# Optimization experiments

Measured on AMD Instinct MI355X. Metric: run time of the kernel, lower is better.

Reference implementation:

```python
import jax, jax.numpy as jnp
import numpy as np

BIG_NEG = -1000000000.0
B, N, X, D = 16, 32, 36, 2048
H = 512

def setup_inputs() -> dict:
    key = jax.random.key(0)
    ks = jax.random.split(key, 16)
    inp = {
        'fc_feats_target': jax.random.normal(ks[0], (B, 1, D), jnp.float32),
        'fc_feats_distr': jax.random.normal(ks[1], (B, N, D), jnp.float32),
        'att_feats_target': jax.random.normal(ks[2], (B, 1, X, D), jnp.float32),
        'att_feats_distr': jax.random.normal(ks[3], (B, N, X, D), jnp.float32),
        'att_masks_target': jax.random.randint(ks[4], (B, 1, X), 0, 2, jnp.int32),
        'att_masks_distr': jax.random.randint(ks[5], (B, N, X), 0, 2, jnp.int32),
        # scorer MLP params: Linear(2D->H), Linear(H->1)
        'W1': jax.random.normal(ks[6], (2 * D, H), jnp.float32) * 0.02,
        'b1': jnp.zeros((H,), jnp.float32),
        'W2': jax.random.normal(ks[7], (H, 1), jnp.float32) * 0.02,
        'b2': jnp.zeros((1,), jnp.float32),
        # bilinear weight, initialized to identity as in the module
        'Wbil': jnp.eye(D, dtype=jnp.float32),
        # object_scorer MLP params
        'oW1': jax.random.normal(ks[8], (2 * D, H), jnp.float32) * 0.02,
        'ob1': jnp.zeros((H,), jnp.float32),
        'oW2': jax.random.normal(ks[9], (H, 1), jnp.float32) * 0.02,
        'ob2': jnp.zeros((1,), jnp.float32),
    }
    return inp

def _mlp(x, W1, b1, W2, b2):
    h = jax.nn.relu(x @ W1 + b1)
    return (h @ W2 + b2)[..., 0]  # squeeze(-1)

def reference(fc_feats_target, fc_feats_distr, att_feats_target, att_feats_distr,
              att_masks_target, att_masks_distr,
              W1, b1, W2, b2, Wbil, oW1, ob1, oW2, ob2):
    # base scorer on global (fc) features
    ft = jnp.broadcast_to(fc_feats_target, fc_feats_distr.shape)  # [B,N,D]
    cat_feats = jnp.concatenate([ft, fc_feats_distr], axis=-1)    # [B,N,2D]
    scores = _mlp(cat_feats, W1, b1, W2, b2)                      # [B,N]

    # bilinear compatibility: einsum('bixd,biye,de->bixy') with target broadcast over i
    tproj = jnp.einsum('bxd,de->bxe', att_feats_target[:, 0], Wbil)        # [B,X,D]
    inners = jnp.einsum('bxd,biyd->bixy', tproj, att_feats_distr)          # [B,N,X,Y]

    mask_outer = (att_masks_target[:, 0][:, None, :, None]
                  * att_masks_distr[:, :, None, :])                        # [B,N,X,Y]
    inners = jnp.where(mask_outer > 0, inners, BIG_NEG)

    target_weights = jax.nn.softmax(jnp.max(inners, axis=3), axis=-1)      # [B,N,X]
    distr_weights = jax.nn.softmax(jnp.max(inners, axis=2), axis=-1)       # [B,N,Y]

    target_feats = jnp.einsum('bxd,bix->bid', att_feats_target[:, 0], target_weights)
    distr_feats = jnp.einsum('biyd,biy->bid', att_feats_distr, distr_weights)

    cat_att = jnp.concatenate([target_feats, distr_feats], axis=-1)        # [B,N,2D]
    scores = scores + _mlp(cat_att, oW1, ob1, oW2, ob2)

    return jax.nn.log_softmax(scores, axis=-1)  # [B,N]
```

## Files before the change

kernel.cpp:

```cpp
#include <hip/hip_runtime.h>
#include <math.h>

#define D_   2048
#define H_   512
#define K2D  4096
#define X_   36
#define NCOL 1152

#define Z_MLP 32
#define Z_TP  8

#define O_A   0u
#define O_B   9437184u
#define O_SB  11534336u
#define O_SO  11534848u
#define O_C   11536384u

typedef __attribute__((ext_vector_type(8))) short bf8_t;
typedef __attribute__((ext_vector_type(4))) float f4_t;

__device__ __forceinline__ unsigned short f2bf(float f) {
  unsigned u = __float_as_uint(f);
  unsigned r = u + 0x7FFFu + ((u >> 16) & 1u);
  return (unsigned short)(r >> 16);
}
__device__ __forceinline__ float bf2f(unsigned short h) {
  return __uint_as_float(((unsigned)h) << 16);
}

#define TSTR 40

__device__ __forceinline__ void cvt8(unsigned short* Hp, unsigned short* Lp,
                                     float4 a, float4 b) {
  __align__(16) unsigned short h[8], l[8];
  float x[8] = {a.x, a.y, a.z, a.w, b.x, b.y, b.z, b.w};
  #pragma unroll
  for (int j = 0; j < 8; j++) {
    h[j] = f2bf(x[j]);
    l[j] = f2bf(x[j] - bf2f(h[j]));
  }
  *(bf8_t*)Hp = *(bf8_t*)&h[0];
  *(bf8_t*)Lp = *(bf8_t*)&l[0];
}

__device__ __forceinline__ void cvt8v(bf8_t* H, bf8_t* L, float4 a, float4 b) {
  float x[8] = {a.x, a.y, a.z, a.w, b.x, b.y, b.z, b.w};
  bf8_t hh, ll;
  #pragma unroll
  for (int j = 0; j < 8; j++) {
    unsigned short h = f2bf(x[j]);
    hh[j] = (short)h;
    ll[j] = (short)f2bf(x[j] - bf2f(h));
  }
  *H = hh; *L = ll;
}

__global__ __launch_bounds__(256, 4) void gemm_mfma64(
    const float* __restrict__ A, const float* __restrict__ A2,
    const float* __restrict__ Bm, float* __restrict__ Cpart,
    int M, int N, int K, int kchunk, int amode)
{
  __shared__ __align__(16) unsigned short AsH[64 * TSTR], AsL[64 * TSTR];
  __shared__ __align__(16) unsigned short BsH[64 * TSTR], BsL[64 * TSTR];
  const int t  = threadIdx.x;
  const int m0 = blockIdx.y << 6;
  const int n0 = blockIdx.x << 6;
  const int k0 = blockIdx.z * kchunk;
  const int kend = k0 + kchunk;
  const int w  = t >> 6;
  const int ln = t & 15;
  const int qd = (t >> 4) & 3;
  const int wm = (w >> 1) << 5;
  const int wn = (w & 1) << 5;
  const int a_row = t >> 2;
  const int a_kq  = (t & 3) << 3;
  const int b_col = t & 63;
  const int b_kq  = (t >> 6) << 3;

  f4_t acc[2][2];
  #pragma unroll
  for (int i = 0; i < 2; i++)
    #pragma unroll
    for (int j = 0; j < 2; j++) acc[i][j] = (f4_t)0.f;

  float4 pa0, pa1;
  float  pb[8];

  auto loadA = [&](int kb) {
    int gr = m0 + a_row;
    int gk = kb + a_kq;
    pa0 = make_float4(0.f, 0.f, 0.f, 0.f);
    pa1 = pa0;
    if (gr < M) {
      const float* src;
      if (amode == 0) src = A + (size_t)gr * K + gk;
      else src = (gk < 2048) ? (A  + ((size_t)(gr >> 5) << 11) + gk)
                             : (A2 + ((size_t)gr << 11) + (gk - 2048));
      pa0 = *(const float4*)src;
      pa1 = *(const float4*)(src + 4);
    }
  };
  auto loadB = [&](int kb) {
    #pragma unroll
    for (int j = 0; j < 8; j++)
      pb[j] = Bm[(size_t)(kb + b_kq + j) * N + n0 + b_col];
  };

  loadA(k0); loadB(k0);

  for (int kb = k0; kb < kend; kb += 32) {
    __syncthreads();
    cvt8(&AsH[a_row * TSTR + a_kq], &AsL[a_row * TSTR + a_kq], pa0, pa1);
    cvt8(&BsH[b_col * TSTR + b_kq], &BsL[b_col * TSTR + b_kq],
         make_float4(pb[0], pb[1], pb[2], pb[3]),
         make_float4(pb[4], pb[5], pb[6], pb[7]));
    __syncthreads();
    if (kb + 32 < kend) { loadA(kb + 32); loadB(kb + 32); }
    bf8_t ah[2], al[2], bh[2], bl[2];
    #pragma unroll
    for (int fm = 0; fm < 2; fm++) {
      int r = (wm + (fm << 4) + ln) * TSTR + (qd << 3);
      ah[fm] = *(const bf8_t*)&AsH[r];
      al[fm] = *(const bf8_t*)&AsL[r];
    }
    #pragma unroll
    for (int fn = 0; fn < 2; fn++) {
      int r = (wn + (fn << 4) + ln) * TSTR + (qd << 3);
      bh[fn] = *(const bf8_t*)&BsH[r];
      bl[fn] = *(const bf8_t*)&BsL[r];
    }
    #pragma unroll
    for (int fm = 0; fm < 2; fm++)
      #pragma unroll
      for (int fn = 0; fn < 2; fn++) {
        acc[fm][fn] = __builtin_amdgcn_mfma_f32_16x16x32_bf16(ah[fm], bh[fn], acc[fm][fn], 0, 0, 0);
        acc[fm][fn] = __builtin_amdgcn_mfma_f32_16x16x32_bf16(ah[fm], bl[fn], acc[fm][fn], 0, 0, 0);
        acc[fm][fn] = __builtin_amdgcn_mfma_f32_16x16x32_bf16(al[fm], bh[fn], acc[fm][fn], 0, 0, 0);
      }
  }
  float* Cz = Cpart + (size_t)blockIdx.z * M * N;
  #pragma unroll
  for (int fm = 0; fm < 2; fm++) {
    #pragma unroll
    for (int reg = 0; reg < 4; reg++) {
      int gr = m0 + wm + (fm << 4) + (qd << 2) + reg;
      if (gr < M) {
        #pragma unroll
        for (int fn = 0; fn < 2; fn++)
          Cz[(size_t)gr * N + n0 + wn + (fn << 4) + ln] = acc[fm][fn][reg];
      }
    }
  }
}

__global__ __launch_bounds__(256) void reduce_tp(
    const float* __restrict__ tpp, unsigned short* __restrict__ tH,
    unsigned short* __restrict__ tL)
{
  int idx = blockIdx.x * 256 + threadIdx.x;
  const float4* p = (const float4*)tpp;
  float4 a = p[idx];
  #pragma unroll
  for (int z = 1; z < Z_TP; z++) {
    float4 b = p[idx + (size_t)z * 294912];
    a.x += b.x; a.y += b.y; a.z += b.z; a.w += b.w;
  }
  ushort4 h, l;
  h.x = f2bf(a.x); l.x = f2bf(a.x - bf2f(h.x));
  h.y = f2bf(a.y); l.y = f2bf(a.y - bf2f(h.y));
  h.z = f2bf(a.z); l.z = f2bf(a.z - bf2f(h.z));
  h.w = f2bf(a.w); l.w = f2bf(a.w - bf2f(h.w));
  ((ushort4*)tH)[idx] = h;
  ((ushort4*)tL)[idx] = l;
}

__global__ __launch_bounds__(256) void mlp_tail_z(
    const float* __restrict__ hp, const float* __restrict__ b1,
    const float* __restrict__ w2, const float* __restrict__ b2,
    float* __restrict__ out)
{
  int row = blockIdx.x;
  int t   = threadIdx.x;
  float v = 0.f;
  #pragma unroll
  for (int q = 0; q < 2; q++) {
    int h = t + (q << 8);
    float s = 0.f;
    #pragma unroll
    for (int z = 0; z < Z_MLP; z++)
      s += hp[(size_t)z * (H_ * 512) + (size_t)row * H_ + h];
    s += b1[h];
    v += fmaxf(s, 0.f) * w2[h];
  }
  #pragma unroll
  for (int off = 32; off > 0; off >>= 1) v += __shfl_down(v, off, 64);
  __shared__ float red[4];
  if ((t & 63) == 0) red[t >> 6] = v;
  __syncthreads();
  if (t == 0) out[row] = red[0] + red[1] + red[2] + red[3] + b2[0];
}

__global__ __launch_bounds__(256, 2) void attn_bi(
    const unsigned short* __restrict__ tH,
    const float* __restrict__ attd,
    const int* __restrict__ amt, const int* __restrict__ amd,
    const float* __restrict__ attt, float* __restrict__ cat)
{
  __shared__ float Sp[4][36][37];
  __shared__ int   mtv[36], mdv[36];
  __shared__ float mrow[36], mcol[36], twl[36], dwl[36];
  const int bi = blockIdx.x;
  const int b  = bi >> 5;
  const int t  = threadIdx.x;
  const int w  = t >> 6;
  const int ln = t & 15;
  const int qd = (t >> 4) & 3;
  if (t < 36) { mtv[t] = amt[b * 36 + t]; mdv[t] = amd[bi * 36 + t]; }

  const unsigned short* tLo = tH + 1179648;
  const int kw = (w << 9) + (qd << 3);
  const unsigned short* AH[3];
  const unsigned short* AL[3];
  const float* BP[3];
  #pragma unroll
  for (int f = 0; f < 3; f++) {
    int r = f * 16 + ln; if (r > 35) r = 35;
    size_t ao = ((size_t)b * X_ + r) * D_ + kw;
    AH[f] = tH  + ao;
    AL[f] = tLo + ao;
    BP[f] = attd + ((size_t)bi * X_ + r) * D_ + kw;
  }

  f4_t acc[3][3];
  #pragma unroll
  for (int i = 0; i < 3; i++)
    #pragma unroll
    for (int j = 0; j < 3; j++) acc[i][j] = (f4_t)0.f;

  bf8_t ah[3], al[3];
  float4 pb0[3], pb1[3];
  #pragma unroll
  for (int f = 0; f < 3; f++) {
    ah[f]  = *(const bf8_t*)AH[f];
    al[f]  = *(const bf8_t*)AL[f];
    pb0[f] = *(const float4*)BP[f];
    pb1[f] = *(const float4*)(BP[f] + 4);
  }

  for (int kk = 0; kk < 16; kk++) {
    bf8_t bh[3], bl[3], cah[3], cal[3];
    #pragma unroll
    for (int f = 0; f < 3; f++) {
      cvt8v(&bh[f], &bl[f], pb0[f], pb1[f]);
      cah[f] = ah[f]; cal[f] = al[f];
    }
    if (kk < 15) {
      const int off = (kk + 1) << 5;
      #pragma unroll
      for (int f = 0; f < 3; f++) {
        ah[f]  = *(const bf8_t*)(AH[f] + off);
        al[f]  = *(const bf8_t*)(AL[f] + off);
        pb0[f] = *(const float4*)(BP[f] + off);
        pb1[f] = *(const float4*)(BP[f] + off + 4);
      }
    }
    #pragma unroll
    for (int fm = 0; fm < 3; fm++)
      #pragma unroll
      for (int fn = 0; fn < 3; fn++) {
        acc[fm][fn] = __builtin_amdgcn_mfma_f32_16x16x32_bf16(cah[fm], bh[fn], acc[fm][fn], 0, 0, 0);
        acc[fm][fn] = __builtin_amdgcn_mfma_f32_16x16x32_bf16(cah[fm], bl[fn], acc[fm][fn], 0, 0, 0);
        acc[fm][fn] = __builtin_amdgcn_mfma_f32_16x16x32_bf16(cal[fm], bh[fn], acc[fm][fn], 0, 0, 0);
      }
  }

  #pragma unroll
  for (int fm = 0; fm < 3; fm++)
    #pragma unroll
    for (int fn = 0; fn < 3; fn++)
      #pragma unroll
      for (int reg = 0; reg < 4; reg++) {
        int x = (fm << 4) + (qd << 2) + reg;
        int y = (fn << 4) + ln;
        if (x < 36 && y < 36) Sp[w][x][y] = acc[fm][fn][reg];
      }
  __syncthreads();
  for (int e = t; e < 1296; e += 256) {
    int x = e / 36, y = e - x * 36;
    float v = Sp[0][x][y] + Sp[1][x][y] + Sp[2][x][y] + Sp[3][x][y];
    Sp[0][x][y] = (mtv[x] != 0 && mdv[y] != 0) ? v : -1e9f;
  }
  __syncthreads();
  if (t < 36) {
    float r = -INFINITY, c = -INFINITY;
    for (int k = 0; k < 36; k++) {
      r = fmaxf(r, Sp[0][t][k]);
      c = fmaxf(c, Sp[0][k][t]);
    }
    mrow[t] = r; mcol[t] = c;
  }
  __syncthreads();
  if (t < 64) {
    float v = (t < 36) ? mrow[t] : -INFINITY;
    float m = v;
    #pragma unroll
    for (int off = 32; off > 0; off >>= 1) m = fmaxf(m, __shfl_xor(m, off, 64));
    float e = (t < 36) ? expf(v - m) : 0.f;
    float s = e;
    #pragma unroll
    for (int off = 32; off > 0; off >>= 1) s += __shfl_xor(s, off, 64);
    if (t < 36) twl[t] = e / s;
  } else if (t < 128) {
    int l = t - 64;
    float v = (l < 36) ? mcol[l] : -INFINITY;
    float m = v;
    #pragma unroll
    for (int off = 32; off > 0; off >>= 1) m = fmaxf(m, __shfl_xor(m, off, 64));
    float e = (l < 36) ? expf(v - m) : 0.f;
    float s = e;
    #pragma unroll
    for (int off = 32; off > 0; off >>= 1) s += __shfl_xor(s, off, 64);
    if (l < 36) dwl[l] = e / s;
  }
  __syncthreads();
  const float4* at4 = (const float4*)(attt + (size_t)b * X_ * D_);
  const float4* ad4 = (const float4*)(attd + (size_t)bi * X_ * D_);
  float4 t0 = make_float4(0, 0, 0, 0), t1 = t0, d0 = t0, d1 = t0;
  for (int x = 0; x < 36; x++) {
    float wt = twl[x], wd = dwl[x];
    float4 a  = at4[x * 512 + t];
    float4 a2 = at4[x * 512 + t + 256];
    float4 e  = ad4[x * 512 + t];
    float4 e2 = ad4[x * 512 + t + 256];
    t0.x = fmaf(wt, a.x, t0.x);  t0.y = fmaf(wt, a.y, t0.y);
    t0.z = fmaf(wt, a.z, t0.z);  t0.w = fmaf(wt, a.w, t0.w);
    t1.x = fmaf(wt, a2.x, t1.x); t1.y = fmaf(wt, a2.y, t1.y);
    t1.z = fmaf(wt, a2.z, t1.z); t1.w = fmaf(wt, a2.w, t1.w);
    d0.x = fmaf(wd, e.x, d0.x);  d0.y = fmaf(wd, e.y, d0.y);
    d0.z = fmaf(wd, e.z, d0.z);  d0.w = fmaf(wd, e.w, d0.w);
    d1.x = fmaf(wd, e2.x, d1.x); d1.y = fmaf(wd, e2.y, d1.y);
    d1.z = fmaf(wd, e2.z, d1.z); d1.w = fmaf(wd, e2.w, d1.w);
  }
  float4* c4 = (float4*)(cat + (size_t)bi * K2D);
  c4[t] = t0; c4[t + 256] = t1; c4[512 + t] = d0; c4[512 + t + 256] = d1;
}

__global__ __launch_bounds__(64) void lsm(
    const float* __restrict__ sb, const float* __restrict__ so,
    float* __restrict__ out)
{
  int b = blockIdx.x, t = threadIdx.x;
  float s = (t < 32) ? sb[b * 32 + t] + so[b * 32 + t] : -INFINITY;
  float m = s;
  #pragma unroll
  for (int off = 32; off > 0; off >>= 1) m = fmaxf(m, __shfl_xor(m, off, 64));
  float e = (t < 32) ? expf(s - m) : 0.f;
  float sum = e;
  #pragma unroll
  for (int off = 32; off > 0; off >>= 1) sum += __shfl_xor(sum, off, 64);
  if (t < 32) out[b * 32 + t] = s - m - logf(sum);
}

extern "C" void kernel_launch(void* const* d_in, const int* in_sizes, int n_in,
                              void* d_out, int out_size, void* d_ws, size_t ws_size,
                              hipStream_t stream)
{
  const float* fc_t  = (const float*)d_in[0];
  const float* fc_d  = (const float*)d_in[1];
  const float* att_t = (const float*)d_in[2];
  const float* att_d = (const float*)d_in[3];
  const int*   am_t  = (const int*)d_in[4];
  const int*   am_d  = (const int*)d_in[5];
  const float* W1    = (const float*)d_in[6];
  const float* b1    = (const float*)d_in[7];
  const float* W2    = (const float*)d_in[8];
  const float* b2    = (const float*)d_in[9];
  const float* Wbil  = (const float*)d_in[10];
  const float* oW1   = (const float*)d_in[11];
  const float* ob1   = (const float*)d_in[12];
  const float* oW2   = (const float*)d_in[13];
  const float* ob2   = (const float*)d_in[14];
  float* ws  = (float*)d_ws;
  float* out = (float*)d_out;

  gemm_mfma64<<<dim3(8, 8, Z_MLP), 256, 0, stream>>>(fc_t, fc_d, W1, ws + O_A,
                                                     512, 512, 4096, 4096 / Z_MLP, 1);
  mlp_tail_z<<<512, 256, 0, stream>>>(ws + O_A, b1, W2, b2, ws + O_SB);
  gemm_mfma64<<<dim3(32, 9, Z_TP), 256, 0, stream>>>(att_t, nullptr, Wbil, ws + O_A,
                                                     576, 2048, 2048, 2048 / Z_TP, 0);
  reduce_tp<<<1152, 256, 0, stream>>>(ws + O_A, (unsigned short*)(ws + O_B),
                                      (unsigned short*)(ws + O_B) + 1179648);
  attn_bi<<<512, 256, 0, stream>>>((const unsigned short*)(ws + O_B), att_d,
                                   am_t, am_d, att_t, ws + O_C);
  gemm_mfma64<<<dim3(8, 8, Z_MLP), 256, 0, stream>>>(ws + O_C, nullptr, oW1, ws + O_A,
                                                     512, 512, 4096, 4096 / Z_MLP, 0);
  mlp_tail_z<<<512, 256, 0, stream>>>(ws + O_A, ob1, oW2, ob2, ws + O_SO);
  lsm<<<16, 64, 0, stream>>>(ws + O_SB, ws + O_SO, out);
}
```

Before: 375.8 us.

## Split attn_bi K-loop across eight waves with 512-thread blocks

Doubles the attn_bi block to 512 threads so eight waves each cover a 256-wide K slice instead of four waves covering 512. The partial score tiles are reduced across eight shared-memory slices, and the weighted-sum phase now gives each thread one float4 per row. The inner loop is also reordered: the A fragments are loaded at the start of each step, and the B prefetch and conversion are interleaved per column fragment. The aim is more memory-level parallelism and latency hiding for a bandwidth-bound kernel, at the cost of more shared memory, a larger cross-wave reduction, and less prefetch of the A operand.

New measurement: 379.5 us. About the same (+1.0%).

```diff
diff --git a/kernel.cpp b/kernel.cpp
--- a/kernel.cpp
+++ b/kernel.cpp
@@ -200,13 +200,13 @@
   if (t == 0) out[row] = red[0] + red[1] + red[2] + red[3] + b2[0];
 }
 
-__global__ __launch_bounds__(256, 2) void attn_bi(
+__global__ __launch_bounds__(512, 4) void attn_bi(
     const unsigned short* __restrict__ tH,
     const float* __restrict__ attd,
     const int* __restrict__ amt, const int* __restrict__ amd,
     const float* __restrict__ attt, float* __restrict__ cat)
 {
-  __shared__ float Sp[4][36][37];
+  __shared__ float Sp[8][36][37];
   __shared__ int   mtv[36], mdv[36];
   __shared__ float mrow[36], mcol[36], twl[36], dwl[36];
   const int bi = blockIdx.x;
@@ -218,7 +218,7 @@
   if (t < 36) { mtv[t] = amt[b * 36 + t]; mdv[t] = amd[bi * 36 + t]; }
 
   const unsigned short* tLo = tH + 1179648;
-  const int kw = (w << 9) + (qd << 3);
+  const int kw = (w << 8) + (qd << 3);
   const unsigned short* AH[3];
   const unsigned short* AL[3];
   const float* BP[3];
@@ -237,41 +237,37 @@
     #pragma unroll
     for (int j = 0; j < 3; j++) acc[i][j] = (f4_t)0.f;
 
-  bf8_t ah[3], al[3];
   float4 pb0[3], pb1[3];
   #pragma unroll
   for (int f = 0; f < 3; f++) {
-    ah[f]  = *(const bf8_t*)AH[f];
-    al[f]  = *(const bf8_t*)AL[f];
     pb0[f] = *(const float4*)BP[f];
     pb1[f] = *(const float4*)(BP[f] + 4);
   }
 
-  for (int kk = 0; kk < 16; kk++) {
-    bf8_t bh[3], bl[3], cah[3], cal[3];
+  for (int kk = 0; kk < 8; kk++) {
+    const int off  = kk << 5;
+    const int noff = (kk + 1) << 5;
+    bf8_t ah[3], al[3];
     #pragma unroll
     for (int f = 0; f < 3; f++) {
-      cvt8v(&bh[f], &bl[f], pb0[f], pb1[f]);
-      cah[f] = ah[f]; cal[f] = al[f];
-    }
-    if (kk < 15) {
-      const int off = (kk + 1) << 5;
+      ah[f] = *(const bf8_t*)(AH[f] + off);
+      al[f] = *(const bf8_t*)(AL[f] + off);
+    }
+    #pragma unroll
+    for (int fn = 0; fn < 3; fn++) {
+      bf8_t bh, bl;
+      cvt8v(&bh, &bl, pb0[fn], pb1[fn]);
+      if (kk < 7) {
+        pb0[fn] = *(const float4*)(BP[fn] + noff);
+        pb1[fn] = *(const float4*)(BP[fn] + noff + 4);
+      }
       #pragma unroll
-      for (int f = 0; f < 3; f++) {
-        ah[f]  = *(const bf8_t*)(AH[f] + off);
-        al[f]  = *(const bf8_t*)(AL[f] + off);
-        pb0[f] = *(const float4*)(BP[f] + off);
-        pb1[f] = *(const float4*)(BP[f] + off + 4);
-      }
-    }
-    #pragma unroll
-    for (int fm = 0; fm < 3; fm++)
-      #pragma unroll
-      for (int fn = 0; fn < 3; fn++) {
-        acc[fm][fn] = __builtin_amdgcn_mfma_f32_16x16x32_bf16(cah[fm], bh[fn], acc[fm][fn], 0, 0, 0);
-        acc[fm][fn] = __builtin_amdgcn_mfma_f32_16x16x32_bf16(cah[fm], bl[fn], acc[fm][fn], 0, 0, 0);
-        acc[fm][fn] = __builtin_amdgcn_mfma_f32_16x16x32_bf16(cal[fm], bh[fn], acc[fm][fn], 0, 0, 0);
-      }
+      for (int fm = 0; fm < 3; fm++) {
+        acc[fm][fn] = __builtin_amdgcn_mfma_f32_16x16x32_bf16(ah[fm], bh, acc[fm][fn], 0, 0, 0);
+        acc[fm][fn] = __builtin_amdgcn_mfma_f32_16x16x32_bf16(ah[fm], bl, acc[fm][fn], 0, 0, 0);
+        acc[fm][fn] = __builtin_amdgcn_mfma_f32_16x16x32_bf16(al[fm], bh, acc[fm][fn], 0, 0, 0);
+      }
+    }
   }
 
   #pragma unroll
@@ -285,9 +281,11 @@
         if (x < 36 && y < 36) Sp[w][x][y] = acc[fm][fn][reg];
       }
   __syncthreads();
-  for (int e = t; e < 1296; e += 256) {
+  for (int e = t; e < 1296; e += 512) {
     int x = e / 36, y = e - x * 36;
-    float v = Sp[0][x][y] + Sp[1][x][y] + Sp[2][x][y] + Sp[3][x][y];
+    float v = Sp[0][x][y];
+    #pragma unroll
+    for (int z = 1; z < 8; z++) v += Sp[z][x][y];
     Sp[0][x][y] = (mtv[x] != 0 && mdv[y] != 0) ? v : -1e9f;
   }
   __syncthreads();
@@ -325,24 +323,18 @@
   __syncthreads();
   const float4* at4 = (const float4*)(attt + (size_t)b * X_ * D_);
   const float4* ad4 = (const float4*)(attd + (size_t)bi * X_ * D_);
-  float4 t0 = make_float4(0, 0, 0, 0), t1 = t0, d0 = t0, d1 = t0;
+  float4 t0 = make_float4(0, 0, 0, 0), d0 = t0;
   for (int x = 0; x < 36; x++) {
     float wt = twl[x], wd = dwl[x];
-    float4 a  = at4[x * 512 + t];
-    float4 a2 = at4[x * 512 + t + 256];
-    float4 e  = ad4[x * 512 + t];
-    float4 e2 = ad4[x * 512 + t + 256];
+    float4 a = at4[x * 512 + t];
+    float4 e = ad4[x * 512 + t];
     t0.x = fmaf(wt, a.x, t0.x);  t0.y = fmaf(wt, a.y, t0.y);
     t0.z = fmaf(wt, a.z, t0.z);  t0.w = fmaf(wt, a.w, t0.w);
-    t1.x = fmaf(wt, a2.x, t1.x); t1.y = fmaf(wt, a2.y, t1.y);
-    t1.z = fmaf(wt, a2.z, t1.z); t1.w = fmaf(wt, a2.w, t1.w);
     d0.x = fmaf(wd, e.x, d0.x);  d0.y = fmaf(wd, e.y, d0.y);
     d0.z = fmaf(wd, e.z, d0.z);  d0.w = fmaf(wd, e.w, d0.w);
-    d1.x = fmaf(wd, e2.x, d1.x); d1.y = fmaf(wd, e2.y, d1.y);
-    d1.z = fmaf(wd, e2.z, d1.z); d1.w = fmaf(wd, e2.w, d1.w);
   }
   float4* c4 = (float4*)(cat + (size_t)bi * K2D);
-  c4[t] = t0; c4[t + 256] = t1; c4[512 + t] = d0; c4[512 + t + 256] = d1;
+  c4[t] = t0; c4[512 + t] = d0;
 }
 
 __global__ __launch_bounds__(64) void lsm(
@@ -390,7 +382,7 @@
                                                      576, 2048, 2048, 2048 / Z_TP, 0);
   reduce_tp<<<1152, 256, 0, stream>>>(ws + O_A, (unsigned short*)(ws + O_B),
                                       (unsigned short*)(ws + O_B) + 1179648);
-  attn_bi<<<512, 256, 0, stream>>>((const unsigned short*)(ws + O_B), att_d,
+  attn_bi<<<512, 512, 0, stream>>>((const unsigned short*)(ws + O_B), att_d,
                                    am_t, am_d, att_t, ws + O_C);
   gemm_mfma64<<<dim3(8, 8, Z_MLP), 256, 0, stream>>>(ws + O_C, nullptr, oW1, ws + O_A,
                                                      512, 512, 4096, 4096 / Z_MLP, 0);
```

## Stage distractor B tiles into LDS via async global_load_lds double buffering

Applied to the files above, without the earlier changes.

The attn_bi kernel now loads the distractor attention-feature tiles with direct global-to-LDS loads into a per-wave double buffer with an XOR swizzle, instead of each lane loading float4 pairs into registers. The FP32-to-bf16 hi/lo split is done per fn fragment from LDS, and fragments are converted and consumed inside the fn loop, which reduces how many B registers are live at once. The aim is fully coalesced 16-byte row loads, overlap of the next tile's fetch with the current tile's MFMAs, and lower register pressure. In exchange it adds LDS usage (about 40KB per block), which can hurt occupancy, and a full vmcnt(0) wait every iteration.

Result: no change. 378.9 us (+0.8%).

```diff
diff --git a/kernel.cpp b/kernel.cpp
--- a/kernel.cpp
+++ b/kernel.cpp
@@ -26,6 +26,12 @@
 }
 __device__ __forceinline__ float bf2f(unsigned short h) {
   return __uint_as_float(((unsigned)h) << 16);
+}
+
+__device__ __forceinline__ void gload16(const void* g, void* l) {
+  __builtin_amdgcn_global_load_lds(
+      (const __attribute__((address_space(1))) unsigned int*)g,
+      (__attribute__((address_space(3))) unsigned int*)l, 16, 0, 0);
 }
 
 #define TSTR 40
@@ -207,29 +213,30 @@
     const float* __restrict__ attt, float* __restrict__ cat)
 {
   __shared__ float Sp[4][36][37];
+  __shared__ __align__(16) float Bs[4][2][1280];
   __shared__ int   mtv[36], mdv[36];
   __shared__ float mrow[36], mcol[36], twl[36], dwl[36];
   const int bi = blockIdx.x;
   const int b  = bi >> 5;
   const int t  = threadIdx.x;
   const int w  = t >> 6;
+  const int lane = t & 63;
   const int ln = t & 15;
   const int qd = (t >> 4) & 3;
   if (t < 36) { mtv[t] = amt[b * 36 + t]; mdv[t] = amd[bi * 36 + t]; }
 
   const unsigned short* tLo = tH + 1179648;
-  const int kw = (w << 9) + (qd << 3);
+  const int kw = w << 9;
   const unsigned short* AH[3];
   const unsigned short* AL[3];
-  const float* BP[3];
   #pragma unroll
   for (int f = 0; f < 3; f++) {
     int r = f * 16 + ln; if (r > 35) r = 35;
-    size_t ao = ((size_t)b * X_ + r) * D_ + kw;
+    size_t ao = ((size_t)b * X_ + r) * D_ + kw + (qd << 3);
     AH[f] = tH  + ao;
     AL[f] = tLo + ao;
-    BP[f] = attd + ((size_t)bi * X_ + r) * D_ + kw;
-  }
+  }
+  const float* Bbase = attd + (size_t)bi * X_ * D_;
 
   f4_t acc[3][3];
   #pragma unroll
@@ -237,41 +244,62 @@
     #pragma unroll
     for (int j = 0; j < 3; j++) acc[i][j] = (f4_t)0.f;
 
+  auto stage = [&](int kk, int cc) {
+    const int k0 = kw + (kk << 5);
+    #pragma unroll
+    for (int j = 0; j < 5; j++) {
+      int r = j * 8 + (lane >> 3); if (r > 35) r = 35;
+      int ss = (lane & 7) ^ (r & 7);
+      gload16(Bbase + (size_t)r * D_ + k0 + (ss << 2), &Bs[w][cc][j << 8]);
+    }
+  };
+
   bf8_t ah[3], al[3];
-  float4 pb0[3], pb1[3];
+  stage(0, 0);
   #pragma unroll
   for (int f = 0; f < 3; f++) {
-    ah[f]  = *(const bf8_t*)AH[f];
-    al[f]  = *(const bf8_t*)AL[f];
-    pb0[f] = *(const float4*)BP[f];
-    pb1[f] = *(const float4*)(BP[f] + 4);
-  }
-
+    ah[f] = *(const bf8_t*)AH[f];
+    al[f] = *(const bf8_t*)AL[f];
+  }
+  asm volatile("s_waitcnt vmcnt(0)" ::: "memory");
+  __builtin_amdgcn_sched_barrier(0);
+
+  int c = 0;
   for (int kk = 0; kk < 16; kk++) {
-    bf8_t bh[3], bl[3], cah[3], cal[3];
-    #pragma unroll
-    for (int f = 0; f < 3; f++) {
-      cvt8v(&bh[f], &bl[f], pb0[f], pb1[f]);
-      cah[f] = ah[f]; cal[f] = al[f];
-    }
+    if (kk < 15) stage(kk + 1, c ^ 1);
+    bf8_t anH[3], anL[3];
     if (kk < 15) {
-      const int off = (kk + 1) << 5;
+      const int o1 = (kk + 1) << 5;
       #pragma unroll
       for (int f = 0; f < 3; f++) {
-        ah[f]  = *(const bf8_t*)(AH[f] + off);
-        al[f]  = *(const bf8_t*)(AL[f] + off);
-        pb0[f] = *(const float4*)(BP[f] + off);
-        pb1[f] = *(const float4*)(BP[f] + off + 4);
+        anH[f] = *(const bf8_t*)(AH[f] + o1);
+        anL[f] = *(const bf8_t*)(AL[f] + o1);
       }
     }
     #pragma unroll
-    for (int fm = 0; fm < 3; fm++)
+    for (int fn = 0; fn < 3; fn++) {
+      int r = fn * 16 + ln; if (r > 35) r = 35;
+      int base = r << 5;
+      int s0 = (((qd << 1)    ) ^ (r & 7)) << 2;
+      int s1 = (((qd << 1) | 1) ^ (r & 7)) << 2;
+      float4 x0 = *(const float4*)&Bs[w][c][base + s0];
+      float4 x1 = *(const float4*)&Bs[w][c][base + s1];
+      bf8_t bh, bl;
+      cvt8v(&bh, &bl, x0, x1);
       #pragma unroll
-      for (int fn = 0; fn < 3; fn++) {
-        acc[fm][fn] = __builtin_amdgcn_mfma_f32_16x16x32_bf16(cah[fm], bh[fn], acc[fm][fn], 0, 0, 0);
-        acc[fm][fn] = __builtin_amdgcn_mfma_f32_16x16x32_bf16(cah[fm], bl[fn], acc[fm][fn], 0, 0, 0);
-        acc[fm][fn] = __builtin_amdgcn_mfma_f32_16x16x32_bf16(cal[fm], bh[fn], acc[fm][fn], 0, 0, 0);
+      for (int fm = 0; fm < 3; fm++) {
+        acc[fm][fn] = __builtin_amdgcn_mfma_f32_16x16x32_bf16(ah[fm], bh, acc[fm][fn], 0, 0, 0);
+        acc[fm][fn] = __builtin_amdgcn_mfma_f32_16x16x32_bf16(ah[fm], bl, acc[fm][fn], 0, 0, 0);
+        acc[fm][fn] = __builtin_amdgcn_mfma_f32_16x16x32_bf16(al[fm], bh, acc[fm][fn], 0, 0, 0);
       }
+    }
+    asm volatile("s_waitcnt vmcnt(0)" ::: "memory");
+    __builtin_amdgcn_sched_barrier(0);
+    c ^= 1;
+    if (kk < 15) {
+      #pragma unroll
+      for (int f = 0; f < 3; f++) { ah[f] = anH[f]; al[f] = anL[f]; }
+    }
   }
 
   #pragma unroll
@@ -292,12 +320,12 @@
   }
   __syncthreads();
   if (t < 36) {
-    float r = -INFINITY, c = -INFINITY;
+    float r = -INFINITY, c2 = -INFINITY;
     for (int k = 0; k < 36; k++) {
-      r = fmaxf(r, Sp[0][t][k]);
-      c = fmaxf(c, Sp[0][k][t]);
-    }
-    mrow[t] = r; mcol[t] = c;
+      r  = fmaxf(r,  Sp[0][t][k]);
+      c2 = fmaxf(c2, Sp[0][k][t]);
+    }
+    mrow[t] = r; mcol[t] = c2;
   }
   __syncthreads();
   if (t < 64) {
```
